# Optimization experiments

Hardware: AMD Instinct MI355X
Metric: run time of the kernel (lower is better)

The kernel has to match this reference:

```python
import jax, jax.numpy as jnp
import numpy as np

B, E, N, D = 32, 16384, 1000, 128


def setup_inputs() -> dict:
    key = jax.random.key(0)
    ks = jax.random.split(key, 8)
    s = 1.0 / np.sqrt(D)
    return {
        "edge_attr": jax.random.normal(ks[0], (B, E, D), dtype=jnp.float32),
        "edge_index": jax.random.randint(ks[1], (B, 2, E), 0, N, dtype=jnp.int32),
        "W1": jax.random.uniform(ks[2], (D, D), jnp.float32, -s, s),
        "b1": jax.random.uniform(ks[3], (D,), jnp.float32, -s, s),
        "W2": jax.random.uniform(ks[4], (D, D), jnp.float32, -s, s),
        "b2": jax.random.uniform(ks[5], (D,), jnp.float32, -s, s),
        "Wo": jax.random.uniform(ks[6], (1, D), jnp.float32, -s, s),
        "bo": jax.random.uniform(ks[7], (1,), jnp.float32, -s, s),
    }


def reference(edge_attr, edge_index, W1, b1, W2, b2, Wo, bo):
    # MLP over edge features: two hidden silu layers then sigmoid output * 10
    h = jax.nn.silu(jnp.einsum("bed,kd->bek", edge_attr, W1) + b1)
    h = jax.nn.silu(jnp.einsum("bed,kd->bek", h, W2) + b2)
    vals = jax.nn.sigmoid(jnp.einsum("bed,kd->bek", h, Wo) + bo)[..., 0] * 10.0  # [B, E]

    src = edge_index[:, 0, :]  # [B, E]
    dst = edge_index[:, 1, :]  # [B, E]
    b_idx = jnp.arange(B, dtype=edge_index.dtype)[:, None]  # [B, 1]
    heat = jnp.zeros((B, N, N), dtype=edge_attr.dtype).at[b_idx, src, dst].set(vals)

    # undirected_graph=True: symmetrize
    return (heat + jnp.swapaxes(heat, 1, 2)) * 0.5
```

## Files before the change

kernel.cpp:

```cpp
#include <hip/hip_runtime.h>
#include <hip/hip_bf16.h>
#include <math.h>

#define B_ 32
#define E_ 16384
#define N_ 1000
#define D_ 128
#define NN_ (N_ * N_)
#define T_ 8

typedef __attribute__((ext_vector_type(8))) short bf16x8;
typedef __attribute__((ext_vector_type(4))) float f32x4;

__device__ __forceinline__ unsigned short f2bf(float f) {
    unsigned u = __float_as_uint(f);
    u += 0x7FFFu + ((u >> 16) & 1u);
    return (unsigned short)(u >> 16);
}

__device__ __forceinline__ unsigned pk2(float lo, float hi) {
    __hip_bfloat162 h = __float22bfloat162_rn(make_float2(lo, hi));
    return *(unsigned*)&h;
}

__device__ __forceinline__ f32x4 mfma16(bf16x8 a, bf16x8 b, f32x4 c) {
    return __builtin_amdgcn_mfma_f32_16x16x32_bf16(a, b, c, 0, 0, 0);
}

__device__ __forceinline__ float silu_(float z) {
    return z * __builtin_amdgcn_rcpf(1.0f + __expf(-z));
}

__device__ __forceinline__ float dec17(unsigned x) {
    return (float)((x & 0x1FFFFu) - 1u) * (10.0f / 131070.0f);
}

__device__ __forceinline__ void gload_lds16(const void* g, void* l) {
    __builtin_amdgcn_global_load_lds(
        (const __attribute__((address_space(1))) unsigned*)g,
        (__attribute__((address_space(3))) unsigned*)l, 16, 0, 0);
}

__global__ __launch_bounds__(256) void fill_zero(uint4* __restrict__ p, int n4) {
    int i = blockIdx.x * 256 + threadIdx.x;
    const int stride = gridDim.x * 256;
    const uint4 z = make_uint4(0u, 0u, 0u, 0u);
    for (; i < n4; i += stride) p[i] = z;
}

__global__ void prep_weights(const float* __restrict__ W1,
                             const float* __restrict__ W2,
                             unsigned short* __restrict__ wsz) {
    int t = blockIdx.x * 256 + threadIdx.x;
    int w = t >> 14, e = t & 16383;
    int row = e >> 7, pos = e & 127;
    int src_col = pos;
    if (w) {
        int q = pos >> 5, gg = (pos >> 3) & 3, nn = (pos >> 2) & 1, r = pos & 3;
        src_col = (q * 2 + nn) * 16 + gg * 4 + r;
    }
    float v = (w ? W2 : W1)[row * 128 + src_col];
    char* dst = (char*)wsz + (size_t)w * 32768 + row * 256 + ((pos * 2) ^ ((row & 7) << 4));
    *(unsigned short*)dst = f2bf(v);
}

__global__ __launch_bounds__(256, 2) void mlp_scatter_kernel(
    const float* __restrict__ X, const int* __restrict__ EI,
    const unsigned short* __restrict__ wsz,
    const float* __restrict__ b1, const float* __restrict__ b2,
    const float* __restrict__ Wo, const float* __restrict__ bo,
    unsigned* __restrict__ out)
{
    __shared__ __align__(16) char Wb[65536];
    __shared__ __align__(16) float BiasL[388];

    const int tid = threadIdx.x;
    const int lane = tid & 63;
    const int wv = tid >> 6;
    const int l15 = lane & 15;
    const int g = (lane >> 4) & 3;

    const int bb = blockIdx.x >> 4;
    const int e0 = (blockIdx.x & 15) * (128 * T_);

    if (tid < 96) {
        const float* src = tid < 32 ? b1 : (tid < 64 ? b2 : Wo);
        ((f32x4*)BiasL)[tid] = ((const f32x4*)src)[tid & 31];
    }
    if (tid == 96) BiasL[384] = bo[0];

    #pragma unroll
    for (int it = 0; it < 16; ++it) {
        int off = it * 4096 + tid * 16;
        gload_lds16((const char*)wsz + off, (char*)Wb + off);
    }
    __syncthreads();
    const float bo0 = BiasL[384];

    #pragma unroll 1
    for (int st = 0; st < T_; ++st) {
        const int eb0 = e0 + st * 128 + wv * 32;

        int eisv[2], eidv[2];
        #pragma unroll
        for (int m = 0; m < 2; ++m) {
            int e = eb0 + m * 16 + l15;
            eisv[m] = EI[(size_t)bb * 2 * E_ + e];
            eidv[m] = EI[(size_t)bb * 2 * E_ + E_ + e];
        }

        bf16x8 a[2][4];
        #pragma unroll
        for (int m = 0; m < 2; ++m) {
            const float* p0 = X + ((size_t)bb * E_ + eb0 + m * 16 + l15) * D_ + g * 8;
            #pragma unroll
            for (int ks = 0; ks < 4; ++ks) {
                float4 u0 = *(const float4*)(p0 + ks * 32);
                float4 u1 = *(const float4*)(p0 + ks * 32 + 4);
                bf16x8 t; unsigned* tu = (unsigned*)&t;
                tu[0] = pk2(u0.x, u0.y); tu[1] = pk2(u0.z, u0.w);
                tu[2] = pk2(u1.x, u1.y); tu[3] = pk2(u1.z, u1.w);
                a[m][ks] = t;
            }
        }

        bf16x8 pa[2][4];
        #pragma unroll
        for (int q = 0; q < 4; ++q) {
            f32x4 acc1[2][2];
            #pragma unroll
            for (int m = 0; m < 2; ++m) {
                acc1[m][0] = (f32x4){0.f, 0.f, 0.f, 0.f};
                acc1[m][1] = (f32x4){0.f, 0.f, 0.f, 0.f};
            }
            #pragma unroll
            for (int ks = 0; ks < 4; ++ks)
                #pragma unroll
                for (int nn = 0; nn < 2; ++nn) {
                    int row = l15 + (q * 2 + nn) * 16;
                    bf16x8 aw = *(const bf16x8*)(Wb + row * 256 +
                                  ((ks * 64 + g * 16) ^ ((row & 7) << 4)));
                    acc1[0][nn] = mfma16(aw, a[0][ks], acc1[0][nn]);
                    acc1[1][nn] = mfma16(aw, a[1][ks], acc1[1][nn]);
                }
            f32x4 b1q0 = ((f32x4*)BiasL)[(q * 2 + 0) * 4 + g];
            f32x4 b1q1 = ((f32x4*)BiasL)[(q * 2 + 1) * 4 + g];
            #pragma unroll
            for (int m = 0; m < 2; ++m) {
                unsigned* au = (unsigned*)&pa[m][q];
                au[0] = pk2(silu_(acc1[m][0][0] + b1q0[0]), silu_(acc1[m][0][1] + b1q0[1]));
                au[1] = pk2(silu_(acc1[m][0][2] + b1q0[2]), silu_(acc1[m][0][3] + b1q0[3]));
                au[2] = pk2(silu_(acc1[m][1][0] + b1q1[0]), silu_(acc1[m][1][1] + b1q1[1]));
                au[3] = pk2(silu_(acc1[m][1][2] + b1q1[2]), silu_(acc1[m][1][3] + b1q1[3]));
            }
            __builtin_amdgcn_sched_barrier(0);
        }

        f32x4 acc2[2][8];
        #pragma unroll
        for (int m = 0; m < 2; ++m)
            #pragma unroll
            for (int n = 0; n < 8; ++n)
                acc2[m][n] = (f32x4){0.f, 0.f, 0.f, 0.f};

        #pragma unroll
        for (int q = 0; q < 4; ++q) {
            #pragma unroll
            for (int n = 0; n < 8; ++n) {
                int row = l15 + n * 16;
                bf16x8 w2 = *(const bf16x8*)(Wb + 32768 + row * 256 +
                              ((q * 64 + g * 16) ^ ((row & 7) << 4)));
                acc2[0][n] = mfma16(w2, pa[0][q], acc2[0][n]);
                acc2[1][n] = mfma16(w2, pa[1][q], acc2[1][n]);
            }
            __builtin_amdgcn_sched_barrier(0);
        }

        float zed[2] = {0.f, 0.f};
        #pragma unroll
        for (int n = 0; n < 8; ++n) {
            f32x4 b2q = ((f32x4*)BiasL)[32 + n * 4 + g];
            f32x4 woq = ((f32x4*)BiasL)[64 + n * 4 + g];
            #pragma unroll
            for (int m = 0; m < 2; ++m) {
                zed[m] += silu_(acc2[m][n][0] + b2q[0]) * woq[0];
                zed[m] += silu_(acc2[m][n][1] + b2q[1]) * woq[1];
                zed[m] += silu_(acc2[m][n][2] + b2q[2]) * woq[2];
                zed[m] += silu_(acc2[m][n][3] + b2q[3]) * woq[3];
            }
        }
        #pragma unroll
        for (int m = 0; m < 2; ++m) {
            zed[m] += __shfl_xor(zed[m], 16, 64);
            zed[m] += __shfl_xor(zed[m], 32, 64);
        }

        if (g == 0) {
            #pragma unroll
            for (int m = 0; m < 2; ++m) {
                int e = eb0 + m * 16 + l15;
                float z = zed[m] + bo0;
                float val = 10.0f * __builtin_amdgcn_rcpf(1.0f + __expf(-z));
                unsigned qv = (unsigned)(val * 13107.0f + 0.5f) + 1u;
                if (qv > 0x1FFFFu) qv = 0x1FFFFu;
                unsigned packed = 0x80000000u | ((unsigned)e << 17) | qv;
                atomicMax(out + ((size_t)bb * NN_ + (size_t)eisv[m] * N_ + eidv[m]),
                          packed);
            }
        }
    }
}

__global__ __launch_bounds__(256) void finalize_fused(
    const int* __restrict__ EI, unsigned* __restrict__ out)
{
    int i = blockIdx.x * 256 + threadIdx.x;
    int b = i >> 14, e = i & 16383;
    int s = EI[(size_t)b * 2 * E_ + e];
    int d = EI[(size_t)b * 2 * E_ + E_ + e];
    unsigned* ob = out + (size_t)b * NN_;
    unsigned x1 = ob[(size_t)s * N_ + d];
    unsigned x2 = ob[(size_t)d * N_ + s];
    float v;
    if (!(x1 >> 31) && x1)      v = __uint_as_float(x1);
    else if (!(x2 >> 31) && x2) v = __uint_as_float(x2);
    else {
        float c1 = (x1 >> 31) ? dec17(x1) : 0.0f;
        float c2 = (x2 >> 31) ? dec17(x2) : 0.0f;
        v = 0.5f * (c1 + c2);
    }
    unsigned uv = __float_as_uint(v);
    ob[(size_t)s * N_ + d] = uv;
    ob[(size_t)d * N_ + s] = uv;
}

extern "C" void kernel_launch(void* const* d_in, const int* in_sizes, int n_in,
                              void* d_out, int out_size, void* d_ws, size_t ws_size,
                              hipStream_t stream) {
    const float* X  = (const float*)d_in[0];
    const int*   EI = (const int*)d_in[1];
    const float* W1 = (const float*)d_in[2];
    const float* b1 = (const float*)d_in[3];
    const float* W2 = (const float*)d_in[4];
    const float* b2 = (const float*)d_in[5];
    const float* Wo = (const float*)d_in[6];
    const float* bo = (const float*)d_in[7];
    unsigned* out = (unsigned*)d_out;
    unsigned short* wsz = (unsigned short*)d_ws;

    fill_zero<<<dim3(2048), dim3(256), 0, stream>>>((uint4*)d_out, out_size / 4);
    prep_weights<<<dim3(128), dim3(256), 0, stream>>>(W1, W2, wsz);
    mlp_scatter_kernel<<<dim3((B_ * E_) / (128 * T_)), dim3(256), 0, stream>>>(
        X, EI, wsz, b1, b2, Wo, bo, out);
    finalize_fused<<<dim3((B_ * E_) / 256), dim3(256), 0, stream>>>(EI, out);
}
```

Before: 146.3 us.

## Prefetch next edge tile, split layer-2 accumulators, merge zero-fill and weight prep

```diff
diff --git a/kernel.cpp b/kernel.cpp
--- a/kernel.cpp
+++ b/kernel.cpp
@@ -41,27 +41,29 @@
         (__attribute__((address_space(3))) unsigned*)l, 16, 0, 0);
 }
 
-__global__ __launch_bounds__(256) void fill_zero(uint4* __restrict__ p, int n4) {
+__global__ __launch_bounds__(256) void fill_and_prep(
+    uint4* __restrict__ p, int n4,
+    const float* __restrict__ W1, const float* __restrict__ W2,
+    unsigned short* __restrict__ wsz)
+{
+    if (blockIdx.x < 128) {
+        int t = blockIdx.x * 256 + threadIdx.x;
+        int w = t >> 14, e = t & 16383;
+        int row = e >> 7, pos = e & 127;
+        int src_col = pos;
+        if (w) {
+            int q = pos >> 5, gg = (pos >> 3) & 3, nn = (pos >> 2) & 1, r = pos & 3;
+            src_col = (q * 2 + nn) * 16 + gg * 4 + r;
+        }
+        float v = (w ? W2 : W1)[row * 128 + src_col];
+        char* dst = (char*)wsz + (size_t)w * 32768 + row * 256 +
+                    ((pos * 2) ^ ((row & 7) << 4));
+        *(unsigned short*)dst = f2bf(v);
+    }
     int i = blockIdx.x * 256 + threadIdx.x;
     const int stride = gridDim.x * 256;
     const uint4 z = make_uint4(0u, 0u, 0u, 0u);
     for (; i < n4; i += stride) p[i] = z;
-}
-
-__global__ void prep_weights(const float* __restrict__ W1,
-                             const float* __restrict__ W2,
-                             unsigned short* __restrict__ wsz) {
-    int t = blockIdx.x * 256 + threadIdx.x;
-    int w = t >> 14, e = t & 16383;
-    int row = e >> 7, pos = e & 127;
-    int src_col = pos;
-    if (w) {
-        int q = pos >> 5, gg = (pos >> 3) & 3, nn = (pos >> 2) & 1, r = pos & 3;
-        src_col = (q * 2 + nn) * 16 + gg * 4 + r;
-    }
-    float v = (w ? W2 : W1)[row * 128 + src_col];
-    char* dst = (char*)wsz + (size_t)w * 32768 + row * 256 + ((pos * 2) ^ ((row & 7) << 4));
-    *(unsigned short*)dst = f2bf(v);
 }
 
 __global__ __launch_bounds__(256, 2) void mlp_scatter_kernel(
@@ -89,6 +91,22 @@
     }
     if (tid == 96) BiasL[384] = bo[0];
 
+    float4 af[2][4][2];
+    auto load_af = [&](int stv) {
+        #pragma unroll
+        for (int m = 0; m < 2; ++m) {
+            const float* p0 = X + ((size_t)bb * E_ + e0 + stv * 128 + wv * 32 +
+                                   m * 16 + l15) * D_ + g * 8;
+            #pragma unroll
+            for (int ks = 0; ks < 4; ++ks) {
+                af[m][ks][0] = *(const float4*)(p0 + ks * 32);
+                af[m][ks][1] = *(const float4*)(p0 + ks * 32 + 4);
+            }
+        }
+    };
+
+    load_af(0);
+
     #pragma unroll
     for (int it = 0; it < 16; ++it) {
         int off = it * 4096 + tid * 16;
@@ -111,18 +129,18 @@
 
         bf16x8 a[2][4];
         #pragma unroll
-        for (int m = 0; m < 2; ++m) {
-            const float* p0 = X + ((size_t)bb * E_ + eb0 + m * 16 + l15) * D_ + g * 8;
+        for (int m = 0; m < 2; ++m)
             #pragma unroll
             for (int ks = 0; ks < 4; ++ks) {
-                float4 u0 = *(const float4*)(p0 + ks * 32);
-                float4 u1 = *(const float4*)(p0 + ks * 32 + 4);
                 bf16x8 t; unsigned* tu = (unsigned*)&t;
-                tu[0] = pk2(u0.x, u0.y); tu[1] = pk2(u0.z, u0.w);
-                tu[2] = pk2(u1.x, u1.y); tu[3] = pk2(u1.z, u1.w);
+                tu[0] = pk2(af[m][ks][0].x, af[m][ks][0].y);
+                tu[1] = pk2(af[m][ks][0].z, af[m][ks][0].w);
+                tu[2] = pk2(af[m][ks][1].x, af[m][ks][1].y);
+                tu[3] = pk2(af[m][ks][1].z, af[m][ks][1].w);
                 a[m][ks] = t;
             }
-        }
+
+        if (st + 1 < T_) load_af(st + 1);
 
         bf16x8 pa[2][4];
         #pragma unroll
@@ -156,39 +174,44 @@
             __builtin_amdgcn_sched_barrier(0);
         }
 
-        f32x4 acc2[2][8];
-        #pragma unroll
-        for (int m = 0; m < 2; ++m)
-            #pragma unroll
-            for (int n = 0; n < 8; ++n)
-                acc2[m][n] = (f32x4){0.f, 0.f, 0.f, 0.f};
-
-        #pragma unroll
-        for (int q = 0; q < 4; ++q) {
-            #pragma unroll
-            for (int n = 0; n < 8; ++n) {
-                int row = l15 + n * 16;
-                bf16x8 w2 = *(const bf16x8*)(Wb + 32768 + row * 256 +
-                              ((q * 64 + g * 16) ^ ((row & 7) << 4)));
-                acc2[0][n] = mfma16(w2, pa[0][q], acc2[0][n]);
-                acc2[1][n] = mfma16(w2, pa[1][q], acc2[1][n]);
-            }
-            __builtin_amdgcn_sched_barrier(0);
-        }
-
         float zed[2] = {0.f, 0.f};
         #pragma unroll
-        for (int n = 0; n < 8; ++n) {
-            f32x4 b2q = ((f32x4*)BiasL)[32 + n * 4 + g];
-            f32x4 woq = ((f32x4*)BiasL)[64 + n * 4 + g];
-            #pragma unroll
-            for (int m = 0; m < 2; ++m) {
-                zed[m] += silu_(acc2[m][n][0] + b2q[0]) * woq[0];
-                zed[m] += silu_(acc2[m][n][1] + b2q[1]) * woq[1];
-                zed[m] += silu_(acc2[m][n][2] + b2q[2]) * woq[2];
-                zed[m] += silu_(acc2[m][n][3] + b2q[3]) * woq[3];
-            }
-        }
+        for (int nh = 0; nh < 2; ++nh) {
+            f32x4 acc2[2][4];
+            #pragma unroll
+            for (int m = 0; m < 2; ++m)
+                #pragma unroll
+                for (int n = 0; n < 4; ++n)
+                    acc2[m][n] = (f32x4){0.f, 0.f, 0.f, 0.f};
+
+            #pragma unroll
+            for (int q = 0; q < 4; ++q) {
+                #pragma unroll
+                for (int n = 0; n < 4; ++n) {
+                    int row = l15 + (nh * 4 + n) * 16;
+                    bf16x8 w2 = *(const bf16x8*)(Wb + 32768 + row * 256 +
+                                  ((q * 64 + g * 16) ^ ((row & 7) << 4)));
+                    acc2[0][n] = mfma16(w2, pa[0][q], acc2[0][n]);
+                    acc2[1][n] = mfma16(w2, pa[1][q], acc2[1][n]);
+                }
+                __builtin_amdgcn_sched_barrier(0);
+            }
+
+            #pragma unroll
+            for (int n = 0; n < 4; ++n) {
+                int nn = nh * 4 + n;
+                f32x4 b2q = ((f32x4*)BiasL)[32 + nn * 4 + g];
+                f32x4 woq = ((f32x4*)BiasL)[64 + nn * 4 + g];
+                #pragma unroll
+                for (int m = 0; m < 2; ++m) {
+                    zed[m] += silu_(acc2[m][n][0] + b2q[0]) * woq[0];
+                    zed[m] += silu_(acc2[m][n][1] + b2q[1]) * woq[1];
+                    zed[m] += silu_(acc2[m][n][2] + b2q[2]) * woq[2];
+                    zed[m] += silu_(acc2[m][n][3] + b2q[3]) * woq[3];
+                }
+            }
+        }
+
         #pragma unroll
         for (int m = 0; m < 2; ++m) {
             zed[m] += __shfl_xor(zed[m], 16, 64);
@@ -248,8 +271,8 @@
     unsigned* out = (unsigned*)d_out;
     unsigned short* wsz = (unsigned short*)d_ws;
 
-    fill_zero<<<dim3(2048), dim3(256), 0, stream>>>((uint4*)d_out, out_size / 4);
-    prep_weights<<<dim3(128), dim3(256), 0, stream>>>(W1, W2, wsz);
+    fill_and_prep<<<dim3(2048), dim3(256), 0, stream>>>(
+        (uint4*)d_out, out_size / 4, W1, W2, wsz);
     mlp_scatter_kernel<<<dim3((B_ * E_) / (128 * T_)), dim3(256), 0, stream>>>(
         X, EI, wsz, b1, b2, Wo, bo, out);
     finalize_fused<<<dim3((B_ * E_) / 256), dim3(256), 0, stream>>>(EI, out);
```

Measured after the change: 143.4 us. No clear change (-2.0%).
